# Kernel optimization log

Hardware: AMD Instinct MI355X
Metric: run time of the kernel (lower is better)

## Reference

```python
import jax, jax.numpy as jnp
import numpy as np

# Bipartite frontier sizes per layer (targets of layer i): fanouts [15,10,5] over 1024 seeds
N_TGT = (60000, 6000, 1024)


def sage_layer(x_src, n_tgt, src, dst, Wl, Wr, b):
    # PyG SAGEConv, aggr='mean', root_weight=True:
    #   out = lin_l(mean_{j in N(i)} x_j) + lin_r(x_i) + bias
    x_tgt = x_src[:n_tgt]                       # [n_tgt, d]
    msg = x_src[src]                            # gather: [E, d]
    agg = jax.ops.segment_sum(msg, dst, num_segments=n_tgt)
    cnt = jax.ops.segment_sum(jnp.ones((src.shape[0], 1), x_src.dtype), dst, num_segments=n_tgt)
    mean = agg / jnp.maximum(cnt, 1.0)          # zero-degree nodes -> 0
    return mean @ Wl + x_tgt @ Wr + b


def setup_inputs() -> dict:
    key = jax.random.key(0)
    ks = jax.random.split(key, 16)
    N0 = 900000
    E = (900000, 60000, 5120)
    dims = [(100, 256), (256, 256), (256, 47)]
    inp = {"x": jax.random.normal(ks[0], (N0, 100), dtype=jnp.float32)}
    n_src = (N0,) + N_TGT[:2]
    for i in range(3):
        inp[f"src{i}"] = jax.random.randint(ks[1 + 2 * i], (E[i],), 0, n_src[i])
        inp[f"dst{i}"] = jax.random.randint(ks[2 + 2 * i], (E[i],), 0, N_TGT[i])
    for i, (din, dout) in enumerate(dims):
        inp[f"Wl{i}"] = jax.random.normal(ks[7 + 3 * i], (din, dout), dtype=jnp.float32) * 0.05
        inp[f"Wr{i}"] = jax.random.normal(ks[8 + 3 * i], (din, dout), dtype=jnp.float32) * 0.05
        inp[f"b{i}"] = jnp.zeros((dout,), dtype=jnp.float32)
    return inp


def reference(x, src0, dst0, src1, dst1, src2, dst2,
              Wl0, Wr0, b0, Wl1, Wr1, b1, Wl2, Wr2, b2):
    srcs = (src0, src1, src2)
    dsts = (dst0, dst1, dst2)
    Wls = (Wl0, Wl1, Wl2)
    Wrs = (Wr0, Wr1, Wr2)
    bs = (b0, b1, b2)
    for i in range(3):
        x = sage_layer(x, N_TGT[i], srcs[i], dsts[i], Wls[i], Wrs[i], bs[i])
        if i != 2:
            x = jax.nn.relu(x)  # dropout is identity in eval mode
    return jax.nn.log_softmax(x, axis=-1)
```

## Files before the change

### kernel.cpp

```cpp
#include <hip/hip_runtime.h>
#include <hip/hip_bf16.h>


typedef short bf16x8 __attribute__((ext_vector_type(8)));
typedef float f32x4 __attribute__((ext_vector_type(4)));

static __device__ __forceinline__ unsigned short f2bf(float f) {
  unsigned u = __float_as_uint(f);
  unsigned r = u + 0x7FFFu + ((u >> 16) & 1u);
  return (unsigned short)(r >> 16);
}
static __device__ __forceinline__ float bf2f_lo(unsigned u) {
  return __uint_as_float(u << 16);
}
static __device__ __forceinline__ float bf2f_hi(unsigned u) {
  return __uint_as_float(u & 0xFFFF0000u);
}
static __device__ __forceinline__ unsigned packbf(float lo, float hi) {
  return ((unsigned)f2bf(hi) << 16) | (unsigned)f2bf(lo);
}

#define E0C 900000
#define E1C 60000
#define E2C 5120
#define ETC 965120
#define HB  3770

#define ROW0_OFF 0
#define ROW1_OFF 60001
#define ROW2_OFF 66002
#define CNT_OFF  67027
#define RANK_OFF 134051
#define SS0_OFF  1099171
#define SS1_OFF  1999171
#define SS2_OFF  2059171
#define TSUM_OFF 2064300

struct TileGeom { int tin, goff, n, tbeg, T; };
static __device__ __forceinline__ TileGeom tile_geom(int b) {
  TileGeom g;
  if (b < 118)      { g.tin = b;       g.goff = 0;     g.n = 60000; g.tbeg = 0;   g.T = 118; }
  else if (b < 130) { g.tin = b - 118; g.goff = 60000; g.n = 6000;  g.tbeg = 118; g.T = 12; }
  else              { g.tin = b - 130; g.goff = 66000; g.n = 1024;  g.tbeg = 130; g.T = 2; }
  return g;
}

__global__ __launch_bounds__(256) void histrank_k(
    const int* __restrict__ d0, const int* __restrict__ d1, const int* __restrict__ d2,
    int* __restrict__ cnt, int* __restrict__ rank) {
  int t = blockIdx.x * 256 + threadIdx.x;
  if (t < E0C) {
    rank[t] = atomicAdd(&cnt[d0[t]], 1);
  } else if (t < E0C + E1C) {
    rank[t] = atomicAdd(&cnt[60000 + d1[t - E0C]], 1);
  } else if (t < ETC) {
    rank[t] = atomicAdd(&cnt[66000 + d2[t - E0C - E1C]], 1);
  }
}

__global__ __launch_bounds__(256) void tilesum_pack_k(
    const int* __restrict__ cnt, int* __restrict__ tsum,
    const float* __restrict__ Wl0, const float* __restrict__ Wr0,
    unsigned short* __restrict__ bm0,
    const float* __restrict__ Wl1, const float* __restrict__ Wr1,
    unsigned short* __restrict__ bm1) {
  const int b = blockIdx.x;
  const int tid = threadIdx.x;
  if (b < 132) {
    __shared__ int red[256];
    const TileGeom g = tile_geom(b);
    const int i0 = g.tin * 512 + 2 * tid;
    int s = 0;
    if (i0 < g.n) s += cnt[g.goff + i0];
    if (i0 + 1 < g.n) s += cnt[g.goff + i0 + 1];
    red[tid] = s;
    __syncthreads();
    for (int off = 128; off; off >>= 1) {
      if (tid < off) red[tid] += red[tid + off];
      __syncthreads();
    }
    if (tid == 0) tsum[b] = red[0];
  } else {
    int j = b - 132;
    int n = tid;
    if (j < 224) {
      int k = j;
      float v = 0.f;
      if (k < 100) v = Wl0[(size_t)k * 256 + n];
      else if (k >= 112 && k < 212) v = Wr0[(size_t)(k - 112) * 256 + n];
      bm0[(((size_t)(k >> 3) * 256) + n) * 8 + (k & 7)] = f2bf(v);
    } else {
      int k = j - 224;
      float v = (k < 256) ? Wl1[(size_t)k * 256 + n] : Wr1[(size_t)(k - 256) * 256 + n];
      bm1[(((size_t)(k >> 3) * 256) + n) * 8 + (k & 7)] = f2bf(v);
    }
  }
}

__global__ __launch_bounds__(256) void scanwrite_k(
    const int* __restrict__ cnt, const int* __restrict__ tsum,
    int* __restrict__ row0, int* __restrict__ row1, int* __restrict__ row2) {
  __shared__ int sc[256];
  const int b = blockIdx.x;
  const TileGeom g = tile_geom(b);
  const int tid = threadIdx.x;
  int* row = (b < 118) ? row0 : (b < 130 ? row1 : row2);

  int p = 0;
  for (int t = g.tbeg + tid; t < b; t += 256) p += tsum[t];
  sc[tid] = p;
  __syncthreads();
  for (int off = 128; off; off >>= 1) {
    if (tid < off) sc[tid] += sc[tid + off];
    __syncthreads();
  }
  const int pref = sc[0];
  __syncthreads();

  const int i0 = g.tin * 512 + 2 * tid;
  const int e0 = (i0 < g.n) ? cnt[g.goff + i0] : 0;
  const int e1 = (i0 + 1 < g.n) ? cnt[g.goff + i0 + 1] : 0;
  sc[tid] = e0 + e1;
  __syncthreads();
  for (int off = 1; off < 256; off <<= 1) {
    int v = (tid >= off) ? sc[tid - off] : 0;
    __syncthreads();
    sc[tid] += v;
    __syncthreads();
  }
  const int excl = sc[tid] - (e0 + e1);
  const int o0 = pref + excl;
  const int o1 = o0 + e0;
  if (i0 < g.n) row[i0] = o0;
  if (i0 + 1 < g.n) row[i0 + 1] = o1;
  if (g.tin == g.T - 1 && tid == 255) row[g.n] = pref + sc[255];
}

__global__ __launch_bounds__(256) void fillscatter_k(
    const int* __restrict__ d0, const int* __restrict__ d1, const int* __restrict__ d2,
    const int* __restrict__ s0, const int* __restrict__ s1, const int* __restrict__ s2,
    const int* __restrict__ row0, const int* __restrict__ row1,
    const int* __restrict__ row2, const int* __restrict__ rank,
    int* __restrict__ o0, int* __restrict__ o1, int* __restrict__ o2) {
  int t = blockIdx.x * 256 + threadIdx.x;
  if (t < E0C) {
    o0[row0[d0[t]] + rank[t]] = s0[t];
  } else if (t < E0C + E1C) {
    int e = t - E0C;
    o1[row1[d1[e]] + rank[t]] = s1[e];
  } else if (t < ETC) {
    int e = t - E0C - E1C;
    o2[row2[d2[e]] + rank[t]] = s2[e];
  }
}

__global__ __launch_bounds__(256) void gather_fused_k(
    const float* __restrict__ x, const int* __restrict__ ss,
    const int* __restrict__ rs, unsigned short* __restrict__ am, int n) {
  int idx = blockIdx.x * 256 + threadIdx.x;
  int w = idx >> 6;
  int f = idx & 63;
  if (w >= n) return;
  const int lo = rs[w];
  const int hi = rs[w + 1];
  float acc0 = 0.f, acc1 = 0.f;
  const int k1 = f + 64;
  int e = lo;
  for (; e + 4 <= hi; e += 4) {
    const float* p0 = x + (size_t)ss[e] * 100;
    const float* p1 = x + (size_t)ss[e + 1] * 100;
    const float* p2 = x + (size_t)ss[e + 2] * 100;
    const float* p3 = x + (size_t)ss[e + 3] * 100;
    acc0 += (p0[f] + p1[f]) + (p2[f] + p3[f]);
    if (k1 < 100) acc1 += (p0[k1] + p1[k1]) + (p2[k1] + p3[k1]);
  }
  for (; e < hi; ++e) {
    const float* p0 = x + (size_t)ss[e] * 100;
    acc0 += p0[f];
    if (k1 < 100) acc1 += p0[k1];
  }
  const float inv = 1.f / (float)max(hi - lo, 1);
  unsigned short* arow = am + (size_t)w * 224;
  arow[f] = f2bf(acc0 * inv);
  if (k1 < 112) arow[k1] = (k1 < 100) ? f2bf(acc1 * inv) : (unsigned short)0;
  const float* xrow = x + (size_t)w * 100;
  arow[112 + f] = f2bf(xrow[f]);
  if (k1 < 112) arow[112 + k1] = (k1 < 100) ? f2bf(xrow[k1]) : (unsigned short)0;
}

__global__ __launch_bounds__(256) void gather_mean_b16_k(
    const unsigned* __restrict__ xbu, const int* __restrict__ ss,
    const int* __restrict__ rs, unsigned* __restrict__ meanu, int n) {
  int idx = blockIdx.x * 256 + threadIdx.x;
  int wp = idx >> 6;
  int f = idx & 63;
  int w = wp >> 1;
  int half = wp & 1;
  if (w >= n) return;
  const int lo = rs[w];
  const int hi = rs[w + 1];
  const int off = half * 64 + f;
  float al = 0.f, ah = 0.f;
  int e = lo;
  for (; e + 4 <= hi; e += 4) {
    unsigned u0 = xbu[(size_t)ss[e] * 128 + off];
    unsigned u1 = xbu[(size_t)ss[e + 1] * 128 + off];
    unsigned u2 = xbu[(size_t)ss[e + 2] * 128 + off];
    unsigned u3 = xbu[(size_t)ss[e + 3] * 128 + off];
    al += (bf2f_lo(u0) + bf2f_lo(u1)) + (bf2f_lo(u2) + bf2f_lo(u3));
    ah += (bf2f_hi(u0) + bf2f_hi(u1)) + (bf2f_hi(u2) + bf2f_hi(u3));
  }
  for (; e < hi; ++e) {
    unsigned u0 = xbu[(size_t)ss[e] * 128 + off];
    al += bf2f_lo(u0);
    ah += bf2f_hi(u0);
  }
  const float inv = 1.f / (float)max(hi - lo, 1);
  meanu[(size_t)w * 128 + off] = packbf(al * inv, ah * inv);
}

__global__ __launch_bounds__(256) void gemm0_k(
    const unsigned short* __restrict__ A, const unsigned short* __restrict__ Bp,
    const float* __restrict__ bias, unsigned short* __restrict__ h0b, int M) {
  constexpr int LDA = 232;
  constexpr int LDC = 264;
  __shared__ unsigned short Sh[64 * LDC];

  const int row0 = blockIdx.x * 64;
  for (int t = threadIdx.x; t < 64 * 28; t += 256) {
    int r = t / 28;
    int c = t - r * 28;
    *reinterpret_cast<uint4*>(&Sh[r * LDA + c * 8]) =
        *reinterpret_cast<const uint4*>(A + (size_t)(row0 + r) * 224 + c * 8);
  }
  __syncthreads();

  const int wid = threadIdx.x >> 6;
  const int l = threadIdx.x & 63;
  const int l15 = l & 15;
  const int lhi = l >> 4;

  f32x4 acc[4][4];
#pragma unroll
  for (int rt = 0; rt < 4; ++rt)
#pragma unroll
    for (int ct = 0; ct < 4; ++ct) acc[rt][ct] = (f32x4){0.f, 0.f, 0.f, 0.f};

  for (int kc = 0; kc < 7; ++kc) {
    bf16x8 a[4], b[4];
#pragma unroll
    for (int rt = 0; rt < 4; ++rt)
      a[rt] = *reinterpret_cast<const bf16x8*>(
          &Sh[(rt * 16 + l15) * LDA + kc * 32 + lhi * 8]);
#pragma unroll
    for (int ct = 0; ct < 4; ++ct) {
      int n = wid * 64 + ct * 16 + l15;
      b[ct] = *reinterpret_cast<const bf16x8*>(
          Bp + ((size_t)(kc * 4 + lhi) * 256 + n) * 8);
    }
#pragma unroll
    for (int rt = 0; rt < 4; ++rt)
#pragma unroll
      for (int ct = 0; ct < 4; ++ct)
        acc[rt][ct] = __builtin_amdgcn_mfma_f32_16x16x32_bf16(a[rt], b[ct],
                                                              acc[rt][ct], 0, 0, 0);
  }
  __syncthreads();

#pragma unroll
  for (int rt = 0; rt < 4; ++rt) {
#pragma unroll
    for (int ct = 0; ct < 4; ++ct) {
      int col = wid * 64 + ct * 16 + l15;
      float bv = bias[col];
#pragma unroll
      for (int r = 0; r < 4; ++r) {
        int rr = rt * 16 + lhi * 4 + r;
        Sh[rr * LDC + col] = f2bf(fmaxf(acc[rt][ct][r] + bv, 0.f));
      }
    }
  }
  __syncthreads();

  const int mrem = M - row0;
  for (int t = threadIdx.x; t < 64 * 32; t += 256) {
    int r = t >> 5;
    int c = t & 31;
    if (r < mrem) {
      *reinterpret_cast<uint4*>(h0b + (size_t)(row0 + r) * 256 + c * 8) =
          *reinterpret_cast<const uint4*>(&Sh[r * LDC + c * 8]);
    }
  }
}

__global__ __launch_bounds__(256) void gemm1_k(
    const unsigned short* __restrict__ A1, const unsigned short* __restrict__ A2,
    const unsigned short* __restrict__ Bp, const float* __restrict__ bias,
    float* __restrict__ h1, int M) {
  constexpr int LDA = 520;
  __shared__ unsigned short As[32 * LDA];

  const int row0 = blockIdx.x * 32;
  for (int t = threadIdx.x; t < 32 * 64; t += 256) {
    int r = t >> 6;
    int c = t & 63;
    const unsigned short* src = (c < 32)
        ? (A1 + (size_t)(row0 + r) * 256 + c * 8)
        : (A2 + (size_t)(row0 + r) * 256 + (c - 32) * 8);
    *reinterpret_cast<uint4*>(&As[r * LDA + c * 8]) =
        *reinterpret_cast<const uint4*>(src);
  }
  __syncthreads();

  const int wid = threadIdx.x >> 6;
  const int l = threadIdx.x & 63;
  const int l15 = l & 15;
  const int lhi = l >> 4;

  f32x4 acc[2][4];
#pragma unroll
  for (int rt = 0; rt < 2; ++rt)
#pragma unroll
    for (int ct = 0; ct < 4; ++ct) acc[rt][ct] = (f32x4){0.f, 0.f, 0.f, 0.f};

  for (int kc = 0; kc < 16; ++kc) {
    bf16x8 a[2], b[4];
#pragma unroll
    for (int rt = 0; rt < 2; ++rt)
      a[rt] = *reinterpret_cast<const bf16x8*>(
          &As[(rt * 16 + l15) * LDA + kc * 32 + lhi * 8]);
#pragma unroll
    for (int ct = 0; ct < 4; ++ct) {
      int n = wid * 64 + ct * 16 + l15;
      b[ct] = *reinterpret_cast<const bf16x8*>(
          Bp + ((size_t)(kc * 4 + lhi) * 256 + n) * 8);
    }
#pragma unroll
    for (int rt = 0; rt < 2; ++rt)
#pragma unroll
      for (int ct = 0; ct < 4; ++ct)
        acc[rt][ct] = __builtin_amdgcn_mfma_f32_16x16x32_bf16(a[rt], b[ct],
                                                              acc[rt][ct], 0, 0, 0);
  }

#pragma unroll
  for (int rt = 0; rt < 2; ++rt) {
#pragma unroll
    for (int ct = 0; ct < 4; ++ct) {
      int col = wid * 64 + ct * 16 + l15;
      float bv = bias[col];
#pragma unroll
      for (int r = 0; r < 4; ++r) {
        int row = row0 + rt * 16 + lhi * 4 + r;
        if (row < M)
          h1[(size_t)row * 256 + col] = fmaxf(acc[rt][ct][r] + bv, 0.f);
      }
    }
  }
}

__global__ __launch_bounds__(256) void final_fused_k(
    const float* __restrict__ h1, const int* __restrict__ ss,
    const int* __restrict__ rs, const float* __restrict__ Wl,
    const float* __restrict__ Wr, const float* __restrict__ bb,
    float* __restrict__ out) {
  __shared__ float sm[4][256];
  __shared__ float sx[4][256];
  const int w = threadIdx.x >> 6;
  const int f = threadIdx.x & 63;
  const int i = blockIdx.x * 4 + w;

  const int lo = rs[i];
  const int hi = rs[i + 1];
  float a0 = 0.f, a1 = 0.f, a2 = 0.f, a3 = 0.f;
  for (int e = lo; e < hi; ++e) {
    const float* p = h1 + (size_t)ss[e] * 256;
    a0 += p[f]; a1 += p[f + 64]; a2 += p[f + 128]; a3 += p[f + 192];
  }
  const float inv = 1.f / (float)max(hi - lo, 1);
  sm[w][f] = a0 * inv; sm[w][f + 64] = a1 * inv;
  sm[w][f + 128] = a2 * inv; sm[w][f + 192] = a3 * inv;
  const float* q = h1 + (size_t)i * 256;
  sx[w][f] = q[f]; sx[w][f + 64] = q[f + 64];
  sx[w][f + 128] = q[f + 128]; sx[w][f + 192] = q[f + 192];

  float acc = -1e30f;
  if (f < 47) {
    float a = bb[f];
    for (int k = 0; k < 256; ++k) {
      a += sm[w][k] * Wl[k * 47 + f] + sx[w][k] * Wr[k * 47 + f];
    }
    acc = a;
  }
  float m = acc;
#pragma unroll
  for (int off = 32; off; off >>= 1) m = fmaxf(m, __shfl_xor(m, off));
  float e2 = (f < 47) ? expf(acc - m) : 0.f;
  float s = e2;
#pragma unroll
  for (int off = 32; off; off >>= 1) s += __shfl_xor(s, off);
  if (f < 47) out[(size_t)i * 47 + f] = acc - m - logf(s);
}

extern "C" void kernel_launch(void* const* d_in, const int* in_sizes, int n_in,
                              void* d_out, int out_size, void* d_ws, size_t ws_size,
                              hipStream_t stream) {
  const float* x    = (const float*)d_in[0];
  const int*   src0 = (const int*)d_in[1];
  const int*   dst0 = (const int*)d_in[2];
  const int*   src1 = (const int*)d_in[3];
  const int*   dst1 = (const int*)d_in[4];
  const int*   src2 = (const int*)d_in[5];
  const int*   dst2 = (const int*)d_in[6];
  const float* Wl0  = (const float*)d_in[7];
  const float* Wr0  = (const float*)d_in[8];
  const float* b0   = (const float*)d_in[9];
  const float* Wl1  = (const float*)d_in[10];
  const float* Wr1  = (const float*)d_in[11];
  const float* b1   = (const float*)d_in[12];
  const float* Wl2  = (const float*)d_in[13];
  const float* Wr2  = (const float*)d_in[14];
  const float* b2   = (const float*)d_in[15];
  float* out = (float*)d_out;

  const int N0 = 60000, N1 = 6000, N2 = 1024;

  char* base = (char*)d_ws;
  unsigned short* bm0  = (unsigned short*)(base);
  unsigned short* bm1  = (unsigned short*)(base + 114688);
  unsigned short* am0  = (unsigned short*)(base + 376832);
  unsigned short* h0b  = (unsigned short*)(base + 27271168);
  unsigned*       h0bu = (unsigned*)(base + 27271168);
  unsigned short* mean1= (unsigned short*)(base + 58007552);
  unsigned*       mean1u=(unsigned*)(base + 58007552);
  float* h1            = (float*)(base + 61087744);
  int* iw              = (int*)(base + 67248128);
  int* row0 = iw + ROW0_OFF;
  int* row1 = iw + ROW1_OFF;
  int* row2 = iw + ROW2_OFF;
  int* cnt  = iw + CNT_OFF;
  int* rank = iw + RANK_OFF;
  int* ss0  = iw + SS0_OFF;
  int* ss1  = iw + SS1_OFF;
  int* ss2  = iw + SS2_OFF;
  int* tsum = iw + TSUM_OFF;

  hipMemsetAsync(cnt, 0, (size_t)67024 * sizeof(int), stream);
  histrank_k<<<HB, 256, 0, stream>>>(dst0, dst1, dst2, cnt, rank);
  tilesum_pack_k<<<132 + 736, 256, 0, stream>>>(cnt, tsum, Wl0, Wr0, bm0,
                                                Wl1, Wr1, bm1);
  scanwrite_k<<<132, 256, 0, stream>>>(cnt, tsum, row0, row1, row2);
  fillscatter_k<<<HB, 256, 0, stream>>>(dst0, dst1, dst2, src0, src1, src2,
                                        row0, row1, row2, rank, ss0, ss1, ss2);

  gather_fused_k<<<(N0 * 64 + 255) / 256, 256, 0, stream>>>(x, ss0, row0, am0, N0);
  gemm0_k<<<(N0 + 63) / 64, 256, 0, stream>>>(am0, bm0, b0, h0b, N0);

  gather_mean_b16_k<<<(N1 * 2 * 64 + 255) / 256, 256, 0, stream>>>(
      h0bu, ss1, row1, mean1u, N1);
  gemm1_k<<<(N1 + 31) / 32, 256, 0, stream>>>(mean1, h0b, bm1, b1, h1, N1);

  final_fused_k<<<N2 / 4, 256, 0, stream>>>(h1, ss2, row2, Wl2, Wr2, b2, out);
}
```

Before: 230.6 us.

## Fuse weight packing into histogram, drop tile-sum pass, enlarge gemm0 row tile

The tile-sum kernel is removed. Its weight-packing blocks are appended to the histogram kernel, and each scan block recomputes its prefix by reading all preceding counts with int4 loads. This removes one launch and one serial dependency, at the cost of redundant count reads in later blocks. gemm0 now processes 96 rows per block instead of 64 to reuse B-fragment loads more, which raises register and LDS use.

```diff
diff --git a/kernel.cpp b/kernel.cpp
--- a/kernel.cpp
+++ b/kernel.cpp
@@ -25,64 +25,46 @@
 #define E2C 5120
 #define ETC 965120
 #define HB  3770
+#define PB  736
 
 #define ROW0_OFF 0
 #define ROW1_OFF 60001
 #define ROW2_OFF 66002
-#define CNT_OFF  67027
-#define RANK_OFF 134051
-#define SS0_OFF  1099171
-#define SS1_OFF  1999171
-#define SS2_OFF  2059171
-#define TSUM_OFF 2064300
-
-struct TileGeom { int tin, goff, n, tbeg, T; };
+#define CNT_OFF  67028
+#define RANK_OFF 134052
+#define SS0_OFF  1099172
+#define SS1_OFF  1999172
+#define SS2_OFF  2059172
+
+struct TileGeom { int tin, goff, n, T; };
 static __device__ __forceinline__ TileGeom tile_geom(int b) {
   TileGeom g;
-  if (b < 118)      { g.tin = b;       g.goff = 0;     g.n = 60000; g.tbeg = 0;   g.T = 118; }
-  else if (b < 130) { g.tin = b - 118; g.goff = 60000; g.n = 6000;  g.tbeg = 118; g.T = 12; }
-  else              { g.tin = b - 130; g.goff = 66000; g.n = 1024;  g.tbeg = 130; g.T = 2; }
+  if (b < 118)      { g.tin = b;       g.goff = 0;     g.n = 60000; g.T = 118; }
+  else if (b < 130) { g.tin = b - 118; g.goff = 60000; g.n = 6000;  g.T = 12; }
+  else              { g.tin = b - 130; g.goff = 66000; g.n = 1024;  g.T = 2; }
   return g;
 }
 
-__global__ __launch_bounds__(256) void histrank_k(
+__global__ __launch_bounds__(256) void histrank_pack_k(
     const int* __restrict__ d0, const int* __restrict__ d1, const int* __restrict__ d2,
-    int* __restrict__ cnt, int* __restrict__ rank) {
-  int t = blockIdx.x * 256 + threadIdx.x;
-  if (t < E0C) {
-    rank[t] = atomicAdd(&cnt[d0[t]], 1);
-  } else if (t < E0C + E1C) {
-    rank[t] = atomicAdd(&cnt[60000 + d1[t - E0C]], 1);
-  } else if (t < ETC) {
-    rank[t] = atomicAdd(&cnt[66000 + d2[t - E0C - E1C]], 1);
-  }
-}
-
-__global__ __launch_bounds__(256) void tilesum_pack_k(
-    const int* __restrict__ cnt, int* __restrict__ tsum,
+    int* __restrict__ cnt, int* __restrict__ rank,
     const float* __restrict__ Wl0, const float* __restrict__ Wr0,
     unsigned short* __restrict__ bm0,
     const float* __restrict__ Wl1, const float* __restrict__ Wr1,
     unsigned short* __restrict__ bm1) {
   const int b = blockIdx.x;
-  const int tid = threadIdx.x;
-  if (b < 132) {
-    __shared__ int red[256];
-    const TileGeom g = tile_geom(b);
-    const int i0 = g.tin * 512 + 2 * tid;
-    int s = 0;
-    if (i0 < g.n) s += cnt[g.goff + i0];
-    if (i0 + 1 < g.n) s += cnt[g.goff + i0 + 1];
-    red[tid] = s;
-    __syncthreads();
-    for (int off = 128; off; off >>= 1) {
-      if (tid < off) red[tid] += red[tid + off];
-      __syncthreads();
-    }
-    if (tid == 0) tsum[b] = red[0];
+  if (b < HB) {
+    int t = b * 256 + threadIdx.x;
+    if (t < E0C) {
+      rank[t] = atomicAdd(&cnt[d0[t]], 1);
+    } else if (t < E0C + E1C) {
+      rank[t] = atomicAdd(&cnt[60000 + d1[t - E0C]], 1);
+    } else if (t < ETC) {
+      rank[t] = atomicAdd(&cnt[66000 + d2[t - E0C - E1C]], 1);
+    }
   } else {
-    int j = b - 132;
-    int n = tid;
+    int j = b - HB;
+    int n = threadIdx.x;
     if (j < 224) {
       int k = j;
       float v = 0.f;
@@ -98,7 +80,7 @@
 }
 
 __global__ __launch_bounds__(256) void scanwrite_k(
-    const int* __restrict__ cnt, const int* __restrict__ tsum,
+    const int* __restrict__ cnt,
     int* __restrict__ row0, int* __restrict__ row1, int* __restrict__ row2) {
   __shared__ int sc[256];
   const int b = blockIdx.x;
@@ -107,7 +89,12 @@
   int* row = (b < 118) ? row0 : (b < 130 ? row1 : row2);
 
   int p = 0;
-  for (int t = g.tbeg + tid; t < b; t += 256) p += tsum[t];
+  const int4* c4 = reinterpret_cast<const int4*>(cnt + g.goff);
+  const int lim4 = (g.tin * 512) >> 2;
+  for (int i = tid; i < lim4; i += 256) {
+    int4 v = c4[i];
+    p += (v.x + v.y) + (v.z + v.w);
+  }
   sc[tid] = p;
   __syncthreads();
   for (int off = 128; off; off >>= 1) {
@@ -224,10 +211,10 @@
     const float* __restrict__ bias, unsigned short* __restrict__ h0b, int M) {
   constexpr int LDA = 232;
   constexpr int LDC = 264;
-  __shared__ unsigned short Sh[64 * LDC];
-
-  const int row0 = blockIdx.x * 64;
-  for (int t = threadIdx.x; t < 64 * 28; t += 256) {
+  __shared__ unsigned short Sh[96 * LDC];
+
+  const int row0 = blockIdx.x * 96;
+  for (int t = threadIdx.x; t < 96 * 28; t += 256) {
     int r = t / 28;
     int c = t - r * 28;
     *reinterpret_cast<uint4*>(&Sh[r * LDA + c * 8]) =
@@ -240,16 +227,16 @@
   const int l15 = l & 15;
   const int lhi = l >> 4;
 
-  f32x4 acc[4][4];
-#pragma unroll
-  for (int rt = 0; rt < 4; ++rt)
+  f32x4 acc[6][4];
+#pragma unroll
+  for (int rt = 0; rt < 6; ++rt)
 #pragma unroll
     for (int ct = 0; ct < 4; ++ct) acc[rt][ct] = (f32x4){0.f, 0.f, 0.f, 0.f};
 
   for (int kc = 0; kc < 7; ++kc) {
-    bf16x8 a[4], b[4];
-#pragma unroll
-    for (int rt = 0; rt < 4; ++rt)
+    bf16x8 a[6], b[4];
+#pragma unroll
+    for (int rt = 0; rt < 6; ++rt)
       a[rt] = *reinterpret_cast<const bf16x8*>(
           &Sh[(rt * 16 + l15) * LDA + kc * 32 + lhi * 8]);
 #pragma unroll
@@ -259,7 +246,7 @@
           Bp + ((size_t)(kc * 4 + lhi) * 256 + n) * 8);
     }
 #pragma unroll
-    for (int rt = 0; rt < 4; ++rt)
+    for (int rt = 0; rt < 6; ++rt)
 #pragma unroll
       for (int ct = 0; ct < 4; ++ct)
         acc[rt][ct] = __builtin_amdgcn_mfma_f32_16x16x32_bf16(a[rt], b[ct],
@@ -268,7 +255,7 @@
   __syncthreads();
 
 #pragma unroll
-  for (int rt = 0; rt < 4; ++rt) {
+  for (int rt = 0; rt < 6; ++rt) {
 #pragma unroll
     for (int ct = 0; ct < 4; ++ct) {
       int col = wid * 64 + ct * 16 + l15;
@@ -283,7 +270,7 @@
   __syncthreads();
 
   const int mrem = M - row0;
-  for (int t = threadIdx.x; t < 64 * 32; t += 256) {
+  for (int t = threadIdx.x; t < 96 * 32; t += 256) {
     int r = t >> 5;
     int c = t & 31;
     if (r < mrem) {
@@ -443,18 +430,16 @@
   int* ss0  = iw + SS0_OFF;
   int* ss1  = iw + SS1_OFF;
   int* ss2  = iw + SS2_OFF;
-  int* tsum = iw + TSUM_OFF;
 
   hipMemsetAsync(cnt, 0, (size_t)67024 * sizeof(int), stream);
-  histrank_k<<<HB, 256, 0, stream>>>(dst0, dst1, dst2, cnt, rank);
-  tilesum_pack_k<<<132 + 736, 256, 0, stream>>>(cnt, tsum, Wl0, Wr0, bm0,
-                                                Wl1, Wr1, bm1);
-  scanwrite_k<<<132, 256, 0, stream>>>(cnt, tsum, row0, row1, row2);
+  histrank_pack_k<<<HB + PB, 256, 0, stream>>>(dst0, dst1, dst2, cnt, rank,
+                                               Wl0, Wr0, bm0, Wl1, Wr1, bm1);
+  scanwrite_k<<<132, 256, 0, stream>>>(cnt, row0, row1, row2);
   fillscatter_k<<<HB, 256, 0, stream>>>(dst0, dst1, dst2, src0, src1, src2,
                                         row0, row1, row2, rank, ss0, ss1, ss2);
 
   gather_fused_k<<<(N0 * 64 + 255) / 256, 256, 0, stream>>>(x, ss0, row0, am0, N0);
-  gemm0_k<<<(N0 + 63) / 64, 256, 0, stream>>>(am0, bm0, b0, h0b, N0);
+  gemm0_k<<<(N0 + 95) / 96, 256, 0, stream>>>(am0, bm0, b0, h0b, N0);
 
   gather_mean_b16_k<<<(N1 * 2 * 64 + 255) / 256, 256, 0, stream>>>(
       h0bu, ss1, row1, mean1u, N1);
```

New measurement: 238.7 us. 1.04x slower.
